# Performance work log

Measured on AMD Instinct MI355X. Metric: run time of the kernel, lower is better.

The kernel has to match this reference:

```python
import jax, jax.numpy as jnp
import numpy as np

D_IN = 2048
N_FEATURES = 16384
K = 32
K_AUX = 256
DEAD_THRESHOLD = 100
N_TOKENS = 4096


def _topk_activation(x, k):
    # relu applied to top-k values, scattered back into zeros (per-row top-k)
    vals, idx = jax.lax.top_k(x, k)            # [B, k]
    vals = jax.nn.relu(vals)
    rows = jnp.arange(x.shape[0])[:, None]
    return jnp.zeros_like(x).at[rows, idx].set(vals)


def setup_inputs() -> dict:
    key = jax.random.key(0)
    ks = jax.random.split(key, 6)
    x = jax.random.normal(ks[0], (N_TOKENS, D_IN), dtype=jnp.float32)
    W_enc = jax.random.normal(ks[1], (D_IN, N_FEATURES), dtype=jnp.float32) * (1.0 / np.sqrt(D_IN))
    b_enc = jax.random.normal(ks[2], (N_FEATURES,), dtype=jnp.float32) * 0.01
    W_dec = jax.random.normal(ks[3], (N_FEATURES, D_IN), dtype=jnp.float32) * (1.0 / np.sqrt(N_FEATURES))
    b_dec = jax.random.normal(ks[4], (D_IN,), dtype=jnp.float32) * 0.01
    steps_since_active = jax.random.randint(ks[5], (N_FEATURES,), 0, 200).astype(jnp.int64)
    return {"x": x, "W_enc": W_enc, "b_enc": b_enc, "W_dec": W_dec,
            "b_dec": b_dec, "steps_since_active": steps_since_active}


def reference(x, W_enc, b_enc, W_dec, b_dec, steps_since_active):
    # encode: linear -> per-row top-k relu sparse activation
    pre = x @ W_enc + b_enc                              # [B, F]
    coeffs = _topk_activation(pre, K)                    # [B, F] sparse (k nnz/row)
    # decode (standard SAE linear decoder)
    recon = coeffs @ W_dec + b_dec                       # [B, D]
    mse = jnp.mean((recon - x) ** 2)
    # dead-feature tracking (buffer update semantics)
    active = jnp.any(jnp.abs(coeffs) > 0, axis=0)        # [F]
    new_steps = jnp.where(active, 0, steps_since_active + 1)
    dead_mask = new_steps >= DEAD_THRESHOLD              # [F]
    # aux loss: top-k over dead features only, fit the residual.
    # Using fixed k=K_AUX is equivalent to k_use=min(K_AUX, n_dead) because
    # relu zeroes the -inf entries picked when fewer than K_AUX features are dead.
    dead_pre = jnp.where(dead_mask[None, :], pre, -jnp.inf)
    aux_coeffs = _topk_activation(dead_pre, K_AUX)       # [B, F]
    residual = x - jax.lax.stop_gradient(recon)
    aux_recon = aux_coeffs @ W_dec + b_dec
    aux = jnp.mean((aux_recon - residual) ** 2)
    loss = mse + aux
    return recon, coeffs, loss, mse, aux
```

## Files before the change

kernel.cpp:

```cpp
#include <hip/hip_runtime.h>

#define NT 4096
#define DIN 2048
#define NF 16384
#define KTOP 32
#define KAUX 256
#define DEAD_TH 100

static constexpr size_t RECON_ELEMS = (size_t)NT * DIN;
static constexpr size_t COEFF_ELEMS = (size_t)NT * NF;

__device__ __forceinline__ unsigned f2k(float f) {
  unsigned b = __float_as_uint(f);
  return (b & 0x80000000u) ? ~b : (b | 0x80000000u);
}
__device__ __forceinline__ float k2f(unsigned k) {
  unsigned b = (k & 0x80000000u) ? (k & 0x7fffffffu) : ~k;
  return __uint_as_float(b);
}

__global__ void k_init(double* sums, int* active) {
  int tid = blockIdx.x * 256 + threadIdx.x;
  if (tid < 2) sums[tid] = 0.0;
  for (int f = tid; f < NF; f += 64 * 256) active[f] = 0;
}

typedef _Float16 h8 __attribute__((ext_vector_type(8)));
typedef float f4 __attribute__((ext_vector_type(4)));

__device__ __forceinline__ void split2(float t0, float t1, unsigned& hi, unsigned& lo) {
  auto h = __builtin_amdgcn_cvt_pkrtz(t0, t1);
  union UH { decltype(h) v; unsigned u; };
  UH uh; uh.v = h; hi = uh.u;
  float r0 = t0 - (float)h.x, r1 = t1 - (float)h.y;
  auto l = __builtin_amdgcn_cvt_pkrtz(r0, r1);
  UH ul; ul.v = l; lo = ul.u;
}

#define BM 128
#define BN 128
#define BK 32

__global__ __launch_bounds__(256, 2) void k_gemm_mfma(const float* __restrict__ A,
                                                      const float* __restrict__ B,
                                                      const float* __restrict__ bias,
                                                      float* __restrict__ C) {
  __shared__ __align__(16) char As_hi[BM * 64];
  __shared__ __align__(16) char As_lo[BM * 64];
  __shared__ __align__(16) char Bs_hi[BN * 64];
  __shared__ __align__(16) char Bs_lo[BN * 64];

  const int tid = threadIdx.x;
  const int lane = tid & 63;
  const int w = tid >> 6;
  const int wm = (w >> 1) * 64, wn = (w & 1) * 64;
  const int row0 = blockIdx.y * BM, col0 = blockIdx.x * BN;

  const float* Ag = A + (size_t)row0 * DIN;
  const float* Bg = B + col0;

  float4 areg[4];
  float breg[2][8];

  f4 acc[4][4];
  #pragma unroll
  for (int i = 0; i < 4; i++)
    #pragma unroll
    for (int j = 0; j < 4; j++) acc[i][j] = (f4){0.f, 0.f, 0.f, 0.f};

  auto loadA = [&](int k0) {
    #pragma unroll
    for (int it = 0; it < 4; it++) {
      int q = it * 256 + tid;
      int m = q >> 3, c4 = q & 7;
      areg[it] = *(const float4*)(Ag + (size_t)m * DIN + k0 + c4 * 4);
    }
  };
  auto loadB = [&](int k0) {
    #pragma unroll
    for (int it = 0; it < 2; it++) {
      int p = it * 256 + tid;
      int n = p & 127, kc = p >> 7;
      const float* bp = Bg + (size_t)(k0 + kc * 8) * NF + n;
      #pragma unroll
      for (int i = 0; i < 8; i++) breg[it][i] = bp[(size_t)i * NF];
    }
  };

  auto convert_write = [&]() {
    #pragma unroll
    for (int it = 0; it < 4; it++) {
      int q = it * 256 + tid;
      int m = q >> 3, c4 = q & 7;
      float4 v = areg[it];
      unsigned h01, l01, h23, l23;
      split2(v.x * 16.f, v.y * 16.f, h01, l01);
      split2(v.z * 16.f, v.w * 16.f, h23, l23);
      unsigned chunk = ((unsigned)c4 >> 1) ^ (((unsigned)m >> 1) & 3u);
      unsigned off = (unsigned)m * 64u + (chunk << 4) + ((unsigned)c4 & 1u) * 8u;
      *(uint2*)(As_hi + off) = make_uint2(h01, h23);
      *(uint2*)(As_lo + off) = make_uint2(l01, l23);
    }
    #pragma unroll
    for (int it = 0; it < 2; it++) {
      int p = it * 256 + tid;
      int n = p & 127, kc = p >> 7;
      unsigned hh[4], ll[4];
      #pragma unroll
      for (int j = 0; j < 4; j++)
        split2(breg[it][2 * j] * 512.f, breg[it][2 * j + 1] * 512.f, hh[j], ll[j]);
      unsigned chunk = (unsigned)kc ^ (((unsigned)n >> 1) & 3u);
      unsigned off = (unsigned)n * 64u + (chunk << 4);
      *(uint4*)(Bs_hi + off) = make_uint4(hh[0], hh[1], hh[2], hh[3]);
      *(uint4*)(Bs_lo + off) = make_uint4(ll[0], ll[1], ll[2], ll[3]);
    }
  };

  auto compute = [&]() {
    const unsigned kchunk = (unsigned)(lane >> 4);
    h8 ah[4], al[4], bh[4], bl[4];
    #pragma unroll
    for (int mt = 0; mt < 4; mt++) {
      unsigned r = (unsigned)(wm + mt * 16 + (lane & 15));
      unsigned off = r * 64u + ((kchunk ^ ((r >> 1) & 3u)) << 4);
      ah[mt] = *(const h8*)(As_hi + off);
      al[mt] = *(const h8*)(As_lo + off);
    }
    #pragma unroll
    for (int nt = 0; nt < 4; nt++) {
      unsigned r = (unsigned)(wn + nt * 16 + (lane & 15));
      unsigned off = r * 64u + ((kchunk ^ ((r >> 1) & 3u)) << 4);
      bh[nt] = *(const h8*)(Bs_hi + off);
      bl[nt] = *(const h8*)(Bs_lo + off);
    }
    #pragma unroll
    for (int mt = 0; mt < 4; mt++)
      #pragma unroll
      for (int nt = 0; nt < 4; nt++) {
        acc[mt][nt] = __builtin_amdgcn_mfma_f32_16x16x32_f16(ah[mt], bh[nt], acc[mt][nt], 0, 0, 0);
        acc[mt][nt] = __builtin_amdgcn_mfma_f32_16x16x32_f16(ah[mt], bl[nt], acc[mt][nt], 0, 0, 0);
        acc[mt][nt] = __builtin_amdgcn_mfma_f32_16x16x32_f16(al[mt], bh[nt], acc[mt][nt], 0, 0, 0);
      }
  };

  loadA(0); loadB(0);
  for (int kt = 0; kt < DIN / BK; kt++) {
    convert_write();
    __syncthreads();
    if (kt + 1 < DIN / BK) { loadA((kt + 1) * BK); loadB((kt + 1) * BK); }
    compute();
    __syncthreads();
  }

  const float inv = 1.0f / 8192.0f;
  #pragma unroll
  for (int nt = 0; nt < 4; nt++) {
    int col = col0 + wn + nt * 16 + (lane & 15);
    float bv = bias[col];
    #pragma unroll
    for (int mt = 0; mt < 4; mt++) {
      int rowb = row0 + wm + mt * 16 + ((lane >> 4) << 2);
      #pragma unroll
      for (int r = 0; r < 4; r++)
        C[(size_t)(rowb + r) * NF + col] = acc[mt][nt][r] * inv + bv;
    }
  }
}

__global__ __launch_bounds__(512, 2) void k_topk(float* __restrict__ pre,
                                                 int* __restrict__ topk_idx,
                                                 float* __restrict__ topk_val,
                                                 int* __restrict__ active) {
  __shared__ __align__(16) float srow[NF];
  __shared__ unsigned hist[8][256];
  __shared__ unsigned redbuf[8];
  __shared__ int sel_idx[KTOP];
  __shared__ float sel_val[KTOP];
  __shared__ unsigned s_prefix;
  __shared__ int s_remaining, s_scnt, s_last;

  const int tid = threadIdx.x;
  const int wv = tid >> 6;
  const int row = blockIdx.x;
  float* rowp = pre + (size_t)row * NF;

  {
    const float4* g4 = (const float4*)rowp;
    float4* s4 = (float4*)srow;
    #pragma unroll
    for (int i = 0; i < 8; i++) s4[i * 512 + tid] = g4[i * 512 + tid];
  }
  if (tid == 0) { s_prefix = 0u; s_remaining = KTOP; s_scnt = 0; }
  __syncthreads();

  const float4* s4 = (const float4*)srow;

  for (int pass = 0; pass < 4; pass++) {
    const int shift = 24 - pass * 8;
    const unsigned mask_hi = pass ? (0xFFFFFFFFu << (shift + 8)) : 0u;
    {
      unsigned* hp = &hist[0][0];
      #pragma unroll
      for (int q = 0; q < 4; q++) hp[q * 512 + tid] = 0;
    }
    __syncthreads();
    const unsigned pfx = s_prefix;
    #pragma unroll
    for (int i = 0; i < 8; i++) {
      float4 v = s4[i * 512 + tid];
      unsigned k0 = f2k(v.x), k1 = f2k(v.y), k2 = f2k(v.z), k3 = f2k(v.w);
      if ((k0 & mask_hi) == pfx) atomicAdd(&hist[wv][(k0 >> shift) & 255u], 1u);
      if ((k1 & mask_hi) == pfx) atomicAdd(&hist[wv][(k1 >> shift) & 255u], 1u);
      if ((k2 & mask_hi) == pfx) atomicAdd(&hist[wv][(k2 >> shift) & 255u], 1u);
      if ((k3 & mask_hi) == pfx) atomicAdd(&hist[wv][(k3 >> shift) & 255u], 1u);
    }
    __syncthreads();
    if (tid < 256) {
      unsigned h = 0;
      #pragma unroll
      for (int w8 = 0; w8 < 8; w8++) h += hist[w8][tid];
      hist[0][tid] = h;
    }
    __syncthreads();
    if (tid == 0) {
      int rem = s_remaining; unsigned above = 0;
      for (int b = 255; b >= 0; b--) {
        unsigned hh = hist[0][b];
        if (above + hh >= (unsigned)rem) {
          s_prefix |= ((unsigned)b) << shift;
          s_remaining = rem - (int)above;
          break;
        }
        above += hh;
      }
    }
    __syncthreads();
  }
  const unsigned T = s_prefix;
  const int r = s_remaining;

  #pragma unroll
  for (int i = 0; i < 8; i++) {
    float4 v = s4[i * 512 + tid];
    const int bidx = (i * 512 + tid) * 4;
    float vv[4] = {v.x, v.y, v.z, v.w};
    #pragma unroll
    for (int e = 0; e < 4; e++) {
      unsigned k = f2k(vv[e]);
      if (k > T) {
        int p = atomicAdd(&s_scnt, 1);
        sel_idx[p] = bidx + e;
        sel_val[p] = vv[e];
      }
    }
  }
  __syncthreads();
  const int cg = s_scnt;
  int last = -1;
  const float tv = k2f(T);
  for (int a = 0; a < r; a++) {
    unsigned mymin = 0xFFFFFFFFu;
    #pragma unroll
    for (int i = 0; i < 8; i++) {
      float4 v = s4[i * 512 + tid];
      const int bidx = (i * 512 + tid) * 4;
      float vv[4] = {v.x, v.y, v.z, v.w};
      #pragma unroll
      for (int e = 0; e < 4; e++) {
        int idx = bidx + e;
        if (f2k(vv[e]) == T && idx > last && (unsigned)idx < mymin) mymin = (unsigned)idx;
      }
    }
    #pragma unroll
    for (int o = 32; o > 0; o >>= 1) {
      unsigned ot = __shfl_down(mymin, o);
      mymin = ot < mymin ? ot : mymin;
    }
    if ((tid & 63) == 0) redbuf[wv] = mymin;
    __syncthreads();
    if (tid == 0) {
      unsigned m = redbuf[0];
      #pragma unroll
      for (int w8 = 1; w8 < 8; w8++) m = redbuf[w8] < m ? redbuf[w8] : m;
      sel_idx[cg + a] = (int)m;
      sel_val[cg + a] = tv;
      s_last = (int)m;
    }
    __syncthreads();
    last = s_last;
  }

  float4 z = {0.f, 0.f, 0.f, 0.f};
  float4* wp4 = (float4*)rowp;
  #pragma unroll
  for (int i = 0; i < 8; i++) wp4[i * 512 + tid] = z;
  __syncthreads();
  if (tid < KTOP) {
    int idx = sel_idx[tid];
    float v = sel_val[tid];
    float c = v > 0.f ? v : 0.f;
    rowp[idx] = c;
    topk_idx[row * KTOP + tid] = idx;
    topk_val[row * KTOP + tid] = c;
    if (v > 0.f) active[idx] = 1;
  }
}

__global__ void k_dead(const int* __restrict__ steps, const int* __restrict__ active,
                       int* __restrict__ dead_idx, int* __restrict__ dead_cnt) {
  __shared__ int cnt[256];
  const int tid = threadIdx.x;
  int c = 0;
  for (int f = tid * 64; f < tid * 64 + 64; f++) {
    int ns = active[f] ? 0 : steps[f] + 1;
    if (ns >= DEAD_TH) c++;
  }
  cnt[tid] = c;
  __syncthreads();
  if (tid == 0) {
    int run = 0;
    for (int t = 0; t < 256; t++) { int x = cnt[t]; cnt[t] = run; run += x; }
    *dead_cnt = run;
  }
  __syncthreads();
  int off = cnt[tid];
  for (int f = tid * 64; f < tid * 64 + 64; f++) {
    int ns = active[f] ? 0 : steps[f] + 1;
    if (ns >= DEAD_TH) dead_idx[off++] = f;
  }
}

__global__ void k_gather(const float* __restrict__ Wenc, const int* __restrict__ dead_idx,
                         const int* __restrict__ dead_cnt, float* __restrict__ w_dead, int Dcap) {
  int D = *dead_cnt; if (D > Dcap) D = Dcap;
  const size_t total = (size_t)D * DIN;
  for (size_t u = (size_t)blockIdx.x * 256 + threadIdx.x; u < total; u += (size_t)gridDim.x * 256) {
    const size_t j = u >> 11, i = u & 2047;
    w_dead[u] = Wenc[i * NF + dead_idx[j]];
  }
}

__global__ __launch_bounds__(256) void k_recon(const float* __restrict__ x, const float* __restrict__ Wdec,
                                               const float* __restrict__ bdec,
                                               const int* __restrict__ topk_idx,
                                               const float* __restrict__ topk_val,
                                               float* __restrict__ recon, double* __restrict__ sums) {
  __shared__ int fidx[KTOP];
  __shared__ float fval[KTOP];
  __shared__ float wred[4];
  const int tid = threadIdx.x, lane = tid & 63, wv = tid >> 6;
  const int row = blockIdx.x;
  if (tid < KTOP) { fidx[tid] = topk_idx[row * KTOP + tid]; fval[tid] = topk_val[row * KTOP + tid]; }
  __syncthreads();
  float4 a0 = {0,0,0,0}, a1 = {0,0,0,0};
  for (int j = 0; j < KTOP; j++) {
    const float c = fval[j];
    if (c > 0.f) {
      const float4* w = (const float4*)(Wdec + (size_t)fidx[j] * DIN);
      float4 w0 = w[tid], w1 = w[256 + tid];
      a0.x = fmaf(c, w0.x, a0.x); a0.y = fmaf(c, w0.y, a0.y);
      a0.z = fmaf(c, w0.z, a0.z); a0.w = fmaf(c, w0.w, a0.w);
      a1.x = fmaf(c, w1.x, a1.x); a1.y = fmaf(c, w1.y, a1.y);
      a1.z = fmaf(c, w1.z, a1.z); a1.w = fmaf(c, w1.w, a1.w);
    }
  }
  const float4* b4 = (const float4*)bdec;
  float4 b0 = b4[tid], b1 = b4[256 + tid];
  float4 r0 = {a0.x + b0.x, a0.y + b0.y, a0.z + b0.z, a0.w + b0.w};
  float4 r1 = {a1.x + b1.x, a1.y + b1.y, a1.z + b1.z, a1.w + b1.w};
  float4* rout = (float4*)(recon + (size_t)row * DIN);
  rout[tid] = r0; rout[256 + tid] = r1;
  const float4* x4 = (const float4*)(x + (size_t)row * DIN);
  float4 x0 = x4[tid], x1 = x4[256 + tid];
  float s = 0.f, d;
  d = r0.x - x0.x; s = fmaf(d, d, s);
  d = r0.y - x0.y; s = fmaf(d, d, s);
  d = r0.z - x0.z; s = fmaf(d, d, s);
  d = r0.w - x0.w; s = fmaf(d, d, s);
  d = r1.x - x1.x; s = fmaf(d, d, s);
  d = r1.y - x1.y; s = fmaf(d, d, s);
  d = r1.z - x1.z; s = fmaf(d, d, s);
  d = r1.w - x1.w; s = fmaf(d, d, s);
  #pragma unroll
  for (int o = 32; o > 0; o >>= 1) s += __shfl_down(s, o);
  if (lane == 0) wred[wv] = s;
  __syncthreads();
  if (tid == 0) {
    double t = (double)wred[0] + (double)wred[1] + (double)wred[2] + (double)wred[3];
    atomicAdd(&sums[0], t);
  }
}

__global__ __launch_bounds__(256) void k_aux(const float* __restrict__ x, const float* __restrict__ Wenc,
                                             const float* __restrict__ benc, const float* __restrict__ Wdec,
                                             const float* __restrict__ bdec, const float* __restrict__ recon,
                                             const int* __restrict__ dead_idx, const int* __restrict__ dead_cnt,
                                             const float* __restrict__ w_dead, int Dcap,
                                             double* __restrict__ sums) {
  __shared__ float xrow[DIN];
  __shared__ unsigned hist[4][256];
  __shared__ int eqj[2048];
  __shared__ int self_[KAUX];
  __shared__ float selc[KAUX];
  __shared__ float wred[4];
  __shared__ unsigned s_prefix;
  __shared__ int s_remaining, s_scnt, s_eqcnt;

  const int tid = threadIdx.x, lane = tid & 63, wv = tid >> 6;
  const int row = blockIdx.x;
  const float4* xg4 = (const float4*)(x + (size_t)row * DIN);
  float4* xr4 = (float4*)xrow;
  xr4[tid] = xg4[tid];
  xr4[256 + tid] = xg4[256 + tid];
  if (tid == 0) { s_prefix = 0u; s_remaining = KAUX; s_scnt = 0; s_eqcnt = 0; }
  __syncthreads();
  const int D = *dead_cnt;

  auto pdval = [&](int jj) -> float {
    const int f = dead_idx[jj];
    float p = 0.f;
    if (jj < Dcap) {
      const float* wd = w_dead + (size_t)jj * DIN;
      for (int i = lane; i < DIN; i += 64) p = fmaf(xrow[i], wd[i], p);
    } else {
      const float* wc = Wenc + f;
      for (int i = lane; i < DIN; i += 64) p = fmaf(xrow[i], wc[(size_t)i * NF], p);
    }
    #pragma unroll
    for (int o = 32; o > 0; o >>= 1) p += __shfl_down(p, o);
    p = __shfl(p, 0);
    return p + benc[f];
  };

  if (D <= KAUX) {
    for (int jj = wv; jj < D; jj += 4) {
      float v = pdval(jj);
      if (lane == 0) { self_[jj] = dead_idx[jj]; selc[jj] = v > 0.f ? v : 0.f; }
    }
    if (tid == 0) s_scnt = D;
    __syncthreads();
  } else {
    for (int pass = 0; pass < 4; pass++) {
      const int shift = 24 - pass * 8;
      const unsigned mask_hi = pass ? (0xFFFFFFFFu << (shift + 8)) : 0u;
      hist[0][tid] = 0; hist[1][tid] = 0; hist[2][tid] = 0; hist[3][tid] = 0;
      __syncthreads();
      const unsigned pfx = s_prefix;
      for (int jj = wv; jj < D; jj += 4) {
        float v = pdval(jj);
        if (lane == 0) {
          unsigned k = f2k(v);
          if ((k & mask_hi) == pfx) atomicAdd(&hist[wv][(k >> shift) & 255u], 1u);
        }
      }
      __syncthreads();
      unsigned h = hist[0][tid] + hist[1][tid] + hist[2][tid] + hist[3][tid];
      hist[0][tid] = h;
      __syncthreads();
      if (tid == 0) {
        int rem = s_remaining; unsigned above = 0;
        for (int b = 255; b >= 0; b--) {
          unsigned hh = hist[0][b];
          if (above + hh >= (unsigned)rem) {
            s_prefix |= ((unsigned)b) << shift;
            s_remaining = rem - (int)above;
            break;
          }
          above += hh;
        }
      }
      __syncthreads();
    }
    const unsigned T = s_prefix;
    const int r = s_remaining;
    for (int jj = wv; jj < D; jj += 4) {
      float v = pdval(jj);
      if (lane == 0) {
        unsigned k = f2k(v);
        if (k > T) { int p = atomicAdd(&s_scnt, 1); self_[p] = dead_idx[jj]; selc[p] = v > 0.f ? v : 0.f; }
        else if (k == T) { int p = atomicAdd(&s_eqcnt, 1); if (p < 2048) eqj[p] = jj; }
      }
    }
    __syncthreads();
    if (tid == 0) {
      int cnt = s_eqcnt < 2048 ? s_eqcnt : 2048;
      const int base = s_scnt;
      const float tv = k2f(T);
      const float tc = tv > 0.f ? tv : 0.f;
      for (int a = 0; a < r; a++) {
        int bestpos = -1, bestj = 0x7fffffff;
        for (int q = 0; q < cnt; q++) { int j = eqj[q]; if (j >= 0 && j < bestj) { bestj = j; bestpos = q; } }
        if (bestpos < 0) break;
        eqj[bestpos] = -1;
        self_[base + a] = dead_idx[bestj];
        selc[base + a] = tc;
      }
      s_scnt = base + r;
    }
    __syncthreads();
  }

  const int scnt = s_scnt;
  float4 a0 = {0,0,0,0}, a1 = {0,0,0,0};
  for (int s = 0; s < scnt; s++) {
    const float c = selc[s];
    if (c > 0.f) {
      const float4* w = (const float4*)(Wdec + (size_t)self_[s] * DIN);
      float4 w0 = w[tid], w1 = w[256 + tid];
      a0.x = fmaf(c, w0.x, a0.x); a0.y = fmaf(c, w0.y, a0.y);
      a0.z = fmaf(c, w0.z, a0.z); a0.w = fmaf(c, w0.w, a0.w);
      a1.x = fmaf(c, w1.x, a1.x); a1.y = fmaf(c, w1.y, a1.y);
      a1.z = fmaf(c, w1.z, a1.z); a1.w = fmaf(c, w1.w, a1.w);
    }
  }
  const float4* b4 = (const float4*)bdec;
  float4 b0 = b4[tid], b1 = b4[256 + tid];
  const float4* rc4 = (const float4*)(recon + (size_t)row * DIN);
  float4 r0 = rc4[tid], r1 = rc4[256 + tid];
  float4 x0 = xr4[tid], x1 = xr4[256 + tid];
  float s = 0.f, d;
  d = (a0.x + b0.x) - (x0.x - r0.x); s = fmaf(d, d, s);
  d = (a0.y + b0.y) - (x0.y - r0.y); s = fmaf(d, d, s);
  d = (a0.z + b0.z) - (x0.z - r0.z); s = fmaf(d, d, s);
  d = (a0.w + b0.w) - (x0.w - r0.w); s = fmaf(d, d, s);
  d = (a1.x + b1.x) - (x1.x - r1.x); s = fmaf(d, d, s);
  d = (a1.y + b1.y) - (x1.y - r1.y); s = fmaf(d, d, s);
  d = (a1.z + b1.z) - (x1.z - r1.z); s = fmaf(d, d, s);
  d = (a1.w + b1.w) - (x1.w - r1.w); s = fmaf(d, d, s);
  #pragma unroll
  for (int o = 32; o > 0; o >>= 1) s += __shfl_down(s, o);
  if (lane == 0) wred[wv] = s;
  __syncthreads();
  if (tid == 0) {
    double t = (double)wred[0] + (double)wred[1] + (double)wred[2] + (double)wred[3];
    atomicAdd(&sums[1], t);
  }
}

__global__ void k_final(const double* __restrict__ sums, float* __restrict__ out_scalars) {
  const double denom = (double)NT * (double)DIN;
  const double mse = sums[0] / denom;
  const double aux = sums[1] / denom;
  out_scalars[0] = (float)(mse + aux);
  out_scalars[1] = (float)mse;
  out_scalars[2] = (float)aux;
}

extern "C" void kernel_launch(void* const* d_in, const int* in_sizes, int n_in,
                              void* d_out, int out_size, void* d_ws, size_t ws_size,
                              hipStream_t stream) {
  const float* x    = (const float*)d_in[0];
  const float* Wenc = (const float*)d_in[1];
  const float* benc = (const float*)d_in[2];
  const float* Wdec = (const float*)d_in[3];
  const float* bdec = (const float*)d_in[4];
  const int*   steps = (const int*)d_in[5];

  float* out = (float*)d_out;
  float* recon   = out;
  float* coeffs  = out + RECON_ELEMS;
  float* scalars = out + RECON_ELEMS + COEFF_ELEMS;

  char* ws = (char*)d_ws;
  size_t off = 0;
  double* sums   = (double*)(ws + off); off += 64;
  int* active    = (int*)(ws + off);    off += (size_t)NF * 4;
  int* dead_cnt  = (int*)(ws + off);    off += 64;
  int* dead_idx  = (int*)(ws + off);    off += (size_t)NF * 4;
  int* topk_idx  = (int*)(ws + off);    off += (size_t)NT * KTOP * 4;
  float* topk_val= (float*)(ws + off);  off += (size_t)NT * KTOP * 4;
  float* w_dead  = (float*)(ws + off);
  int Dcap = 0;
  if (ws_size > off) {
    size_t cap = (ws_size - off) / ((size_t)DIN * 4);
    Dcap = cap > 1024 ? 1024 : (int)cap;
  }

  k_init<<<64, 256, 0, stream>>>(sums, active);
  dim3 gemm_grid(NF / BN, NT / BM);
  k_gemm_mfma<<<gemm_grid, 256, 0, stream>>>(x, Wenc, benc, coeffs);
  k_topk<<<NT, 512, 0, stream>>>(coeffs, topk_idx, topk_val, active);
  k_dead<<<1, 256, 0, stream>>>(steps, active, dead_idx, dead_cnt);
  k_gather<<<256, 256, 0, stream>>>(Wenc, dead_idx, dead_cnt, w_dead, Dcap);
  k_recon<<<NT, 256, 0, stream>>>(x, Wdec, bdec, topk_idx, topk_val, recon, sums);
  k_aux<<<NT, 256, 0, stream>>>(x, Wenc, benc, Wdec, bdec, recon, dead_idx, dead_cnt, w_dead, Dcap, sums);
  k_final<<<1, 1, 0, stream>>>(sums, scalars);
}
```

Before: 1.945 ms.

## Pre-split GEMM operands to fp16 hi/lo and use candidate-filtered radix top-k

Adds pre-pass kernels that convert x and a transposed W_enc into fp16 hi/lo pairs in workspace, so the encoder GEMM streams half-precision tiles instead of converting fp32 inside the main loop. The recon output buffer is reused as scratch for the split x. The top-k kernel drops the full-row shared-memory copy: it runs a first-byte histogram from global memory, then gathers the boundary bucket into a small candidate list and runs the remaining radix passes on that list only. This depends on the workspace being large enough and adds extra passes over W_enc plus a transposed write of it.

Result: slower. 4.143 ms (+113.0%).

```diff
diff --git a/kernel.cpp b/kernel.cpp
--- a/kernel.cpp
+++ b/kernel.cpp
@@ -37,9 +37,145 @@
   UH ul; ul.v = l; lo = ul.u;
 }
 
+__global__ void k_splitA(const float* __restrict__ A, ushort* __restrict__ hi,
+                         ushort* __restrict__ lo) {
+  size_t u = ((size_t)blockIdx.x * 256 + threadIdx.x) * 8;
+  float4 v0 = *(const float4*)(A + u), v1 = *(const float4*)(A + u + 4);
+  unsigned h[4], l[4];
+  split2(v0.x * 16.f, v0.y * 16.f, h[0], l[0]);
+  split2(v0.z * 16.f, v0.w * 16.f, h[1], l[1]);
+  split2(v1.x * 16.f, v1.y * 16.f, h[2], l[2]);
+  split2(v1.z * 16.f, v1.w * 16.f, h[3], l[3]);
+  *(uint4*)(hi + u) = make_uint4(h[0], h[1], h[2], h[3]);
+  *(uint4*)(lo + u) = make_uint4(l[0], l[1], l[2], l[3]);
+}
+
+__global__ void k_splitB(const float* __restrict__ B, ushort* __restrict__ bthi,
+                         ushort* __restrict__ btlo) {
+  const int n = blockIdx.x * 256 + threadIdx.x;
+  const int k0 = blockIdx.y * 32;
+  float v[32];
+  #pragma unroll
+  for (int i = 0; i < 32; i++) v[i] = B[(size_t)(k0 + i) * NF + n] * 512.f;
+  unsigned h[16], l[16];
+  #pragma unroll
+  for (int j = 0; j < 16; j++) split2(v[2 * j], v[2 * j + 1], h[j], l[j]);
+  ushort* dh = bthi + (size_t)n * DIN + k0;
+  ushort* dl = btlo + (size_t)n * DIN + k0;
+  #pragma unroll
+  for (int q = 0; q < 4; q++) {
+    *(uint4*)(dh + q * 8) = make_uint4(h[4 * q], h[4 * q + 1], h[4 * q + 2], h[4 * q + 3]);
+    *(uint4*)(dl + q * 8) = make_uint4(l[4 * q], l[4 * q + 1], l[4 * q + 2], l[4 * q + 3]);
+  }
+}
+
 #define BM 128
 #define BN 128
 #define BK 32
+
+__global__ __launch_bounds__(256, 2) void k_gemm_pre(const ushort* __restrict__ Ahi,
+                                                     const ushort* __restrict__ Alo,
+                                                     const ushort* __restrict__ Bthi,
+                                                     const ushort* __restrict__ Btlo,
+                                                     const float* __restrict__ bias,
+                                                     float* __restrict__ C) {
+  __shared__ __align__(16) char As_hi[BM * 64];
+  __shared__ __align__(16) char As_lo[BM * 64];
+  __shared__ __align__(16) char Bs_hi[BN * 64];
+  __shared__ __align__(16) char Bs_lo[BN * 64];
+
+  const int tid = threadIdx.x;
+  const int lane = tid & 63;
+  const int w = tid >> 6;
+  const int wm = (w >> 1) * 64, wn = (w & 1) * 64;
+  const int row0 = blockIdx.y * BM, col0 = blockIdx.x * BN;
+
+  const int srow = tid >> 2;
+  const int schunk = tid & 3;
+
+  uint4 sAh[2], sAl[2], sBh[2], sBl[2];
+
+  f4 acc[4][4];
+  #pragma unroll
+  for (int i = 0; i < 4; i++)
+    #pragma unroll
+    for (int j = 0; j < 4; j++) acc[i][j] = (f4){0.f, 0.f, 0.f, 0.f};
+
+  auto loadT = [&](int k0) {
+    #pragma unroll
+    for (int it = 0; it < 2; it++) {
+      int r = it * 64 + srow;
+      size_t abyte = ((size_t)(row0 + r) * DIN + k0) * 2 + (size_t)schunk * 16;
+      size_t bbyte = ((size_t)(col0 + r) * DIN + k0) * 2 + (size_t)schunk * 16;
+      sAh[it] = *(const uint4*)((const char*)Ahi + abyte);
+      sAl[it] = *(const uint4*)((const char*)Alo + abyte);
+      sBh[it] = *(const uint4*)((const char*)Bthi + bbyte);
+      sBl[it] = *(const uint4*)((const char*)Btlo + bbyte);
+    }
+  };
+  auto writeT = [&]() {
+    #pragma unroll
+    for (int it = 0; it < 2; it++) {
+      int r = it * 64 + srow;
+      unsigned pc = (unsigned)schunk ^ (((unsigned)r >> 1) & 3u);
+      unsigned off = (unsigned)r * 64u + (pc << 4);
+      *(uint4*)(As_hi + off) = sAh[it];
+      *(uint4*)(As_lo + off) = sAl[it];
+      *(uint4*)(Bs_hi + off) = sBh[it];
+      *(uint4*)(Bs_lo + off) = sBl[it];
+    }
+  };
+
+  auto compute = [&]() {
+    const unsigned kchunk = (unsigned)(lane >> 4);
+    h8 ah[4], al[4], bh[4], bl[4];
+    #pragma unroll
+    for (int mt = 0; mt < 4; mt++) {
+      unsigned r = (unsigned)(wm + mt * 16 + (lane & 15));
+      unsigned off = r * 64u + ((kchunk ^ ((r >> 1) & 3u)) << 4);
+      ah[mt] = *(const h8*)(As_hi + off);
+      al[mt] = *(const h8*)(As_lo + off);
+    }
+    #pragma unroll
+    for (int nt = 0; nt < 4; nt++) {
+      unsigned r = (unsigned)(wn + nt * 16 + (lane & 15));
+      unsigned off = r * 64u + ((kchunk ^ ((r >> 1) & 3u)) << 4);
+      bh[nt] = *(const h8*)(Bs_hi + off);
+      bl[nt] = *(const h8*)(Bs_lo + off);
+    }
+    #pragma unroll
+    for (int mt = 0; mt < 4; mt++)
+      #pragma unroll
+      for (int nt = 0; nt < 4; nt++) {
+        acc[mt][nt] = __builtin_amdgcn_mfma_f32_16x16x32_f16(ah[mt], bh[nt], acc[mt][nt], 0, 0, 0);
+        acc[mt][nt] = __builtin_amdgcn_mfma_f32_16x16x32_f16(ah[mt], bl[nt], acc[mt][nt], 0, 0, 0);
+        acc[mt][nt] = __builtin_amdgcn_mfma_f32_16x16x32_f16(al[mt], bh[nt], acc[mt][nt], 0, 0, 0);
+      }
+  };
+
+  loadT(0);
+  for (int kt = 0; kt < DIN / BK; kt++) {
+    writeT();
+    __syncthreads();
+    if (kt + 1 < DIN / BK) loadT((kt + 1) * BK);
+    compute();
+    __syncthreads();
+  }
+
+  const float inv = 1.0f / 8192.0f;
+  #pragma unroll
+  for (int nt = 0; nt < 4; nt++) {
+    int col = col0 + wn + nt * 16 + (lane & 15);
+    float bv = bias[col];
+    #pragma unroll
+    for (int mt = 0; mt < 4; mt++) {
+      int rowb = row0 + wm + mt * 16 + ((lane >> 4) << 2);
+      #pragma unroll
+      for (int r = 0; r < 4; r++)
+        C[(size_t)(rowb + r) * NF + col] = acc[mt][nt][r] * inv + bv;
+    }
+  }
+}
 
 __global__ __launch_bounds__(256, 2) void k_gemm_mfma(const float* __restrict__ A,
                                                       const float* __restrict__ B,
@@ -167,129 +303,262 @@
   }
 }
 
-__global__ __launch_bounds__(512, 2) void k_topk(float* __restrict__ pre,
-                                                 int* __restrict__ topk_idx,
-                                                 float* __restrict__ topk_val,
-                                                 int* __restrict__ active) {
-  __shared__ __align__(16) float srow[NF];
+#define CAND 4096
+__global__ __launch_bounds__(512) void k_topk(float* __restrict__ pre,
+                                              int* __restrict__ topk_idx,
+                                              float* __restrict__ topk_val,
+                                              int* __restrict__ active) {
   __shared__ unsigned hist[8][256];
+  __shared__ int cand_idx[CAND];
+  __shared__ unsigned cand_key[CAND];
   __shared__ unsigned redbuf[8];
   __shared__ int sel_idx[KTOP];
   __shared__ float sel_val[KTOP];
   __shared__ unsigned s_prefix;
-  __shared__ int s_remaining, s_scnt, s_last;
+  __shared__ int s_remaining, s_scnt, s_ccnt, s_bcnt, s_last;
 
   const int tid = threadIdx.x;
   const int wv = tid >> 6;
   const int row = blockIdx.x;
   float* rowp = pre + (size_t)row * NF;
-
+  const float4* g4 = (const float4*)rowp;
+
+  if (tid == 0) { s_scnt = 0; s_ccnt = 0; }
   {
-    const float4* g4 = (const float4*)rowp;
-    float4* s4 = (float4*)srow;
-    #pragma unroll
-    for (int i = 0; i < 8; i++) s4[i * 512 + tid] = g4[i * 512 + tid];
-  }
-  if (tid == 0) { s_prefix = 0u; s_remaining = KTOP; s_scnt = 0; }
-  __syncthreads();
-
-  const float4* s4 = (const float4*)srow;
-
-  for (int pass = 0; pass < 4; pass++) {
-    const int shift = 24 - pass * 8;
-    const unsigned mask_hi = pass ? (0xFFFFFFFFu << (shift + 8)) : 0u;
-    {
-      unsigned* hp = &hist[0][0];
-      #pragma unroll
-      for (int q = 0; q < 4; q++) hp[q * 512 + tid] = 0;
-    }
-    __syncthreads();
-    const unsigned pfx = s_prefix;
-    #pragma unroll
-    for (int i = 0; i < 8; i++) {
-      float4 v = s4[i * 512 + tid];
-      unsigned k0 = f2k(v.x), k1 = f2k(v.y), k2 = f2k(v.z), k3 = f2k(v.w);
-      if ((k0 & mask_hi) == pfx) atomicAdd(&hist[wv][(k0 >> shift) & 255u], 1u);
-      if ((k1 & mask_hi) == pfx) atomicAdd(&hist[wv][(k1 >> shift) & 255u], 1u);
-      if ((k2 & mask_hi) == pfx) atomicAdd(&hist[wv][(k2 >> shift) & 255u], 1u);
-      if ((k3 & mask_hi) == pfx) atomicAdd(&hist[wv][(k3 >> shift) & 255u], 1u);
-    }
-    __syncthreads();
-    if (tid < 256) {
-      unsigned h = 0;
-      #pragma unroll
-      for (int w8 = 0; w8 < 8; w8++) h += hist[w8][tid];
-      hist[0][tid] = h;
-    }
-    __syncthreads();
-    if (tid == 0) {
-      int rem = s_remaining; unsigned above = 0;
-      for (int b = 255; b >= 0; b--) {
-        unsigned hh = hist[0][b];
-        if (above + hh >= (unsigned)rem) {
-          s_prefix |= ((unsigned)b) << shift;
-          s_remaining = rem - (int)above;
-          break;
-        }
-        above += hh;
-      }
-    }
-    __syncthreads();
-  }
-  const unsigned T = s_prefix;
-  const int r = s_remaining;
-
+    unsigned* hp = &hist[0][0];
+    #pragma unroll
+    for (int q = 0; q < 4; q++) hp[q * 512 + tid] = 0;
+  }
+  __syncthreads();
   #pragma unroll
   for (int i = 0; i < 8; i++) {
-    float4 v = s4[i * 512 + tid];
+    float4 v = g4[i * 512 + tid];
+    atomicAdd(&hist[wv][f2k(v.x) >> 24], 1u);
+    atomicAdd(&hist[wv][f2k(v.y) >> 24], 1u);
+    atomicAdd(&hist[wv][f2k(v.z) >> 24], 1u);
+    atomicAdd(&hist[wv][f2k(v.w) >> 24], 1u);
+  }
+  __syncthreads();
+  if (tid < 256) {
+    unsigned h = 0;
+    #pragma unroll
+    for (int w8 = 0; w8 < 8; w8++) h += hist[w8][tid];
+    hist[0][tid] = h;
+  }
+  __syncthreads();
+  if (tid == 0) {
+    unsigned above = 0; int rem = KTOP;
+    for (int b = 255; b >= 0; b--) {
+      unsigned hh = hist[0][b];
+      if (above + hh >= (unsigned)rem) {
+        s_prefix = ((unsigned)b) << 24;
+        s_remaining = rem - (int)above;
+        s_bcnt = (int)hh;
+        break;
+      }
+      above += hh;
+    }
+  }
+  __syncthreads();
+  const unsigned b0 = s_prefix >> 24;
+  const int bcnt = s_bcnt;
+
+  #pragma unroll
+  for (int i = 0; i < 8; i++) {
+    float4 v = g4[i * 512 + tid];
     const int bidx = (i * 512 + tid) * 4;
     float vv[4] = {v.x, v.y, v.z, v.w};
     #pragma unroll
     for (int e = 0; e < 4; e++) {
       unsigned k = f2k(vv[e]);
-      if (k > T) {
+      unsigned b = k >> 24;
+      if (b > b0) {
         int p = atomicAdd(&s_scnt, 1);
         sel_idx[p] = bidx + e;
         sel_val[p] = vv[e];
-      }
-    }
-  }
-  __syncthreads();
-  const int cg = s_scnt;
-  int last = -1;
-  const float tv = k2f(T);
-  for (int a = 0; a < r; a++) {
-    unsigned mymin = 0xFFFFFFFFu;
+      } else if (b == b0 && bcnt <= CAND) {
+        int p = atomicAdd(&s_ccnt, 1);
+        cand_idx[p] = bidx + e;
+        cand_key[p] = k;
+      }
+    }
+  }
+  __syncthreads();
+
+  if (bcnt <= CAND) {
+    const int ccnt = s_ccnt;
+    for (int pass = 1; pass < 4; pass++) {
+      const int shift = 24 - pass * 8;
+      const unsigned mask_hi = 0xFFFFFFFFu << (shift + 8);
+      {
+        unsigned* hp = &hist[0][0];
+        #pragma unroll
+        for (int q = 0; q < 4; q++) hp[q * 512 + tid] = 0;
+      }
+      __syncthreads();
+      const unsigned pfx = s_prefix;
+      for (int c = tid; c < ccnt; c += 512) {
+        unsigned k = cand_key[c];
+        if ((k & mask_hi) == pfx) atomicAdd(&hist[wv][(k >> shift) & 255u], 1u);
+      }
+      __syncthreads();
+      if (tid < 256) {
+        unsigned h = 0;
+        #pragma unroll
+        for (int w8 = 0; w8 < 8; w8++) h += hist[w8][tid];
+        hist[0][tid] = h;
+      }
+      __syncthreads();
+      if (tid == 0) {
+        int rem = s_remaining; unsigned above = 0;
+        for (int b = 255; b >= 0; b--) {
+          unsigned hh = hist[0][b];
+          if (above + hh >= (unsigned)rem) {
+            s_prefix |= ((unsigned)b) << shift;
+            s_remaining = rem - (int)above;
+            break;
+          }
+          above += hh;
+        }
+      }
+      __syncthreads();
+    }
+    const unsigned T = s_prefix;
+    const int r = s_remaining;
+    for (int c = tid; c < ccnt; c += 512) {
+      unsigned k = cand_key[c];
+      if (k > T) {
+        int p = atomicAdd(&s_scnt, 1);
+        sel_idx[p] = cand_idx[c];
+        sel_val[p] = k2f(k);
+      }
+    }
+    __syncthreads();
+    const int cg = s_scnt;
+    int last = -1;
+    const float tv = k2f(T);
+    for (int a = 0; a < r; a++) {
+      unsigned mymin = 0xFFFFFFFFu;
+      for (int c = tid; c < ccnt; c += 512) {
+        if (cand_key[c] == T) {
+          int idx = cand_idx[c];
+          if (idx > last && (unsigned)idx < mymin) mymin = (unsigned)idx;
+        }
+      }
+      #pragma unroll
+      for (int o = 32; o > 0; o >>= 1) {
+        unsigned ot = __shfl_down(mymin, o);
+        mymin = ot < mymin ? ot : mymin;
+      }
+      if ((tid & 63) == 0) redbuf[wv] = mymin;
+      __syncthreads();
+      if (tid == 0) {
+        unsigned m = redbuf[0];
+        #pragma unroll
+        for (int w8 = 1; w8 < 8; w8++) m = redbuf[w8] < m ? redbuf[w8] : m;
+        sel_idx[cg + a] = (int)m;
+        sel_val[cg + a] = tv;
+        s_last = (int)m;
+      }
+      __syncthreads();
+      last = s_last;
+    }
+  } else {
+    for (int pass = 1; pass < 4; pass++) {
+      const int shift = 24 - pass * 8;
+      const unsigned mask_hi = 0xFFFFFFFFu << (shift + 8);
+      {
+        unsigned* hp = &hist[0][0];
+        #pragma unroll
+        for (int q = 0; q < 4; q++) hp[q * 512 + tid] = 0;
+      }
+      __syncthreads();
+      const unsigned pfx = s_prefix;
+      #pragma unroll
+      for (int i = 0; i < 8; i++) {
+        float4 v = g4[i * 512 + tid];
+        unsigned kk[4] = {f2k(v.x), f2k(v.y), f2k(v.z), f2k(v.w)};
+        #pragma unroll
+        for (int e = 0; e < 4; e++)
+          if ((kk[e] & mask_hi) == pfx) atomicAdd(&hist[wv][(kk[e] >> shift) & 255u], 1u);
+      }
+      __syncthreads();
+      if (tid < 256) {
+        unsigned h = 0;
+        #pragma unroll
+        for (int w8 = 0; w8 < 8; w8++) h += hist[w8][tid];
+        hist[0][tid] = h;
+      }
+      __syncthreads();
+      if (tid == 0) {
+        int rem = s_remaining; unsigned above = 0;
+        for (int b = 255; b >= 0; b--) {
+          unsigned hh = hist[0][b];
+          if (above + hh >= (unsigned)rem) {
+            s_prefix |= ((unsigned)b) << shift;
+            s_remaining = rem - (int)above;
+            break;
+          }
+          above += hh;
+        }
+      }
+      __syncthreads();
+    }
+    const unsigned T = s_prefix;
+    const int r = s_remaining;
     #pragma unroll
     for (int i = 0; i < 8; i++) {
-      float4 v = s4[i * 512 + tid];
+      float4 v = g4[i * 512 + tid];
       const int bidx = (i * 512 + tid) * 4;
       float vv[4] = {v.x, v.y, v.z, v.w};
       #pragma unroll
       for (int e = 0; e < 4; e++) {
-        int idx = bidx + e;
-        if (f2k(vv[e]) == T && idx > last && (unsigned)idx < mymin) mymin = (unsigned)idx;
-      }
-    }
-    #pragma unroll
-    for (int o = 32; o > 0; o >>= 1) {
-      unsigned ot = __shfl_down(mymin, o);
-      mymin = ot < mymin ? ot : mymin;
-    }
-    if ((tid & 63) == 0) redbuf[wv] = mymin;
+        unsigned k = f2k(vv[e]);
+        if ((k >> 24) == b0 && k > T) {
+          int p = atomicAdd(&s_scnt, 1);
+          sel_idx[p] = bidx + e;
+          sel_val[p] = vv[e];
+        }
+      }
+    }
     __syncthreads();
-    if (tid == 0) {
-      unsigned m = redbuf[0];
-      #pragma unroll
-      for (int w8 = 1; w8 < 8; w8++) m = redbuf[w8] < m ? redbuf[w8] : m;
-      sel_idx[cg + a] = (int)m;
-      sel_val[cg + a] = tv;
-      s_last = (int)m;
-    }
-    __syncthreads();
-    last = s_last;
-  }
-
+    const int cg = s_scnt;
+    int last = -1;
+    const float tv = k2f(T);
+    for (int a = 0; a < r; a++) {
+      unsigned mymin = 0xFFFFFFFFu;
+      #pragma unroll
+      for (int i = 0; i < 8; i++) {
+        float4 v = g4[i * 512 + tid];
+        const int bidx = (i * 512 + tid) * 4;
+        float vv[4] = {v.x, v.y, v.z, v.w};
+        #pragma unroll
+        for (int e = 0; e < 4; e++) {
+          int idx = bidx + e;
+          if (f2k(vv[e]) == T && idx > last && (unsigned)idx < mymin) mymin = (unsigned)idx;
+        }
+      }
+      #pragma unroll
+      for (int o = 32; o > 0; o >>= 1) {
+        unsigned ot = __shfl_down(mymin, o);
+        mymin = ot < mymin ? ot : mymin;
+      }
+      if ((tid & 63) == 0) redbuf[wv] = mymin;
+      __syncthreads();
+      if (tid == 0) {
+        unsigned m = redbuf[0];
+        #pragma unroll
+        for (int w8 = 1; w8 < 8; w8++) m = redbuf[w8] < m ? redbuf[w8] : m;
+        sel_idx[cg + a] = (int)m;
+        sel_val[cg + a] = tv;
+        s_last = (int)m;
+      }
+      __syncthreads();
+      last = s_last;
+    }
+  }
+
+  __syncthreads();
   float4 z = {0.f, 0.f, 0.f, 0.f};
   float4* wp4 = (float4*)rowp;
   #pragma unroll
@@ -569,6 +838,15 @@
   int* dead_idx  = (int*)(ws + off);    off += (size_t)NF * 4;
   int* topk_idx  = (int*)(ws + off);    off += (size_t)NT * KTOP * 4;
   float* topk_val= (float*)(ws + off);  off += (size_t)NT * KTOP * 4;
+
+  const size_t bt_elems = (size_t)DIN * NF;
+  bool pre = false;
+  ushort *Bthi = nullptr, *Btlo = nullptr;
+  if (ws_size >= off + bt_elems * 4 + (size_t)128 * DIN * 4) {
+    Bthi = (ushort*)(ws + off); off += bt_elems * 2;
+    Btlo = (ushort*)(ws + off); off += bt_elems * 2;
+    pre = true;
+  }
   float* w_dead  = (float*)(ws + off);
   int Dcap = 0;
   if (ws_size > off) {
@@ -576,9 +854,18 @@
     Dcap = cap > 1024 ? 1024 : (int)cap;
   }
 
+  ushort* Ahi = (ushort*)recon;
+  ushort* Alo = Ahi + RECON_ELEMS;
+
   k_init<<<64, 256, 0, stream>>>(sums, active);
   dim3 gemm_grid(NF / BN, NT / BM);
-  k_gemm_mfma<<<gemm_grid, 256, 0, stream>>>(x, Wenc, benc, coeffs);
+  if (pre) {
+    k_splitA<<<4096, 256, 0, stream>>>(x, Ahi, Alo);
+    k_splitB<<<dim3(64, 64), 256, 0, stream>>>(Wenc, Bthi, Btlo);
+    k_gemm_pre<<<gemm_grid, 256, 0, stream>>>(Ahi, Alo, Bthi, Btlo, benc, coeffs);
+  } else {
+    k_gemm_mfma<<<gemm_grid, 256, 0, stream>>>(x, Wenc, benc, coeffs);
+  }
   k_topk<<<NT, 512, 0, stream>>>(coeffs, topk_idx, topk_val, active);
   k_dead<<<1, 256, 0, stream>>>(steps, active, dead_idx, dead_cnt);
   k_gather<<<256, 256, 0, stream>>>(Wenc, dead_idx, dead_cnt, w_dead, Dcap);
```
